# Kernel tuning notes

Hardware: AMD Instinct MI355X
Metric: run time of the kernel (lower is better)

Reference implementation:

```python
import jax, jax.numpy as jnp
import numpy as np

ROUTING_ITERS = 3
EPS = 1e-8

def _squash_elem(s):
    # Faithful to torch squash with dim=-1 over a trailing size-1 axis: elementwise.
    sq = s * s
    return (sq / (1.0 + sq)) * s / jnp.sqrt(sq + EPS)

def setup_inputs() -> dict:
    key = jax.random.key(0)
    k1, k2 = jax.random.split(key)
    x = jax.random.normal(k1, (64, 1152, 64), dtype=jnp.float32)            # [B, N_routes, in_ch]
    route_weights = jax.random.normal(k2, (32, 1152, 64, 64), dtype=jnp.float32)  # [C, N, out, in]
    return {"x": x, "route_weights": route_weights}

def reference(x, route_weights):
    B = x.shape[0]
    C, N, O, _ = route_weights.shape
    # u_hat: [B, C, N, O]  (torch trailing size-1 dim dropped; squash/sums over it are elementwise)
    u_hat = jnp.einsum('cnoi,bni->bcno', route_weights, x)
    b_ij = jnp.zeros((B, C, N, 1), dtype=x.dtype)
    v_j = None
    for i in range(ROUTING_ITERS):
        c_ij = jax.nn.softmax(b_ij, axis=1)                  # over capsules
        s_j = jnp.sum(c_ij * u_hat, axis=2, keepdims=True)   # [B, C, 1, O]
        v_j = _squash_elem(s_j)
        if i < ROUTING_ITERS - 1:
            # torch: b_ij + (u_hat * v_j).sum(-1, keepdim) over size-1 dim -> broadcasts to [B,C,N,O]
            b_ij = b_ij + u_hat * v_j
    return v_j[:, :, 0, :]  # [B, C, O]
```

## Files before the change

kernel.cpp:

```cpp
#include <hip/hip_runtime.h>
#include <hip/hip_bf16.h>

typedef short short8v __attribute__((ext_vector_type(8)));
typedef float float4v __attribute__((ext_vector_type(4)));

constexpr int Bb = 64;
constexpr int Cc = 32;
constexpr int Nn = 1152;
constexpr int Oo = 64;
constexpr int Ii = 64;
constexpr int NCH = 32;
constexpr int CHN = 36;
constexpr int OT  = 16;

__device__ __forceinline__ unsigned short bf16_rne(float f) {
    unsigned u = __float_as_uint(f);
    u += 0x7FFFu + ((u >> 16) & 1u);
    return (unsigned short)(u >> 16);
}
__device__ __forceinline__ float bf16_f(unsigned short h) {
    return __uint_as_float(((unsigned)h) << 16);
}
__device__ __forceinline__ float squash_elem(float s) {
    float sq = s * s;
    return (sq / (1.f + sq)) * s / sqrtf(sq + 1e-8f);
}

__device__ __forceinline__ void barrier_nodrain() {
    asm volatile("s_waitcnt lgkmcnt(0)" ::: "memory");
    __builtin_amdgcn_s_barrier();
    asm volatile("" ::: "memory");
}

__device__ __forceinline__ void split8(const float4& f0, const float4& f1,
                                       short8v& h, short8v& lo) {
    float a[8] = {f0.x, f0.y, f0.z, f0.w, f1.x, f1.y, f1.z, f1.w};
#pragma unroll
    for (int e = 0; e < 8; ++e) {
        unsigned short hb = bf16_rne(a[e]);
        h[e] = (short)hb;
        lo[e] = (short)bf16_rne(a[e] - bf16_f(hb));
    }
}

__global__ __launch_bounds__(256) void prep_xt(const float* __restrict__ x,
                                               unsigned short* __restrict__ xh,
                                               unsigned short* __restrict__ xl) {
    const int n = blockIdx.x, t = threadIdx.x;
    const int b = t >> 2, q = t & 3;
    const float* src = x + ((size_t)b * Nn + n) * Ii + q * 16;
    float4 v0 = *(const float4*)(src);
    float4 v1 = *(const float4*)(src + 4);
    float4 v2 = *(const float4*)(src + 8);
    float4 v3 = *(const float4*)(src + 12);
    short8v h0, l0, h1, l1;
    split8(v0, v1, h0, l0);
    split8(v2, v3, h1, l1);
    size_t dst = (size_t)n * (Bb * Ii) + b * Ii + q * 16;
    *(short8v*)(xh + dst) = h0;
    *(short8v*)(xh + dst + 8) = h1;
    *(short8v*)(xl + dst) = l0;
    *(short8v*)(xl + dst + 8) = l1;
}

template <int MODE>
__global__ __launch_bounds__(256, 2) void caps_pass(
    const float* __restrict__ w, const unsigned short* __restrict__ xh,
    const unsigned short* __restrict__ xl, const float* __restrict__ V,
    float* __restrict__ part) {
    __shared__ unsigned short sh[2][128 * 64];
    __shared__ unsigned short sl[2][128 * 64];

    const int t = threadIdx.x;
    const int l = t & 63, wv = t >> 6;
    const int ch = blockIdx.x, ot = blockIdx.y;
    const int obase = ot * 4;
    const int kg = l >> 4;
    const int lm = l & 15;
    const int n0 = ch * CHN;
    const int sw = (lm & 7) << 3;

    float Vreg[8][4];
    if constexpr (MODE == 1) {
#pragma unroll
        for (int t8 = 0; t8 < 8; ++t8)
#pragma unroll
            for (int r = 0; r < 4; ++r) {
                int b = 16 * wv + 4 * kg + r;
                int c = 4 * t8 + ((l >> 2) & 3);
                int o = obase + (l & 3);
                Vreg[t8][r] = V[((size_t)b * Cc + c) * Oo + o];
            }
    }
    float4v acc4[8];
    float accs[8][4];
#pragma unroll
    for (int t8 = 0; t8 < 8; ++t8) {
        acc4[t8] = (float4v){0.f, 0.f, 0.f, 0.f};
#pragma unroll
        for (int r = 0; r < 4; ++r) accs[t8][r] = 0.f;
    }

    const int i0 = (t & 15) * 4;
    const int colb = t >> 4;
    float4 L0[8], L1[8];

    auto issue = [&](int n, float4(&ld)[8]) {
#pragma unroll
        for (int k = 0; k < 8; ++k) {
            int col = colb + 16 * k;
            int c = col >> 2, olc = col & 3;
            ld[k] = *(const float4*)(
                w + (((size_t)c * Nn + n) * Oo + obase + olc) * Ii + i0);
        }
    };
    auto writebuf = [&](unsigned short* dh, unsigned short* dl,
                        const float4(&ld)[8]) {
#pragma unroll
        for (int k = 0; k < 8; ++k) {
            int col = colb + 16 * k;
            int off = col * 64 + (i0 ^ ((col & 7) << 3));
            short8v H, Lo;
            split8(ld[k], *(const float4*)nullptr == *(const float4*)nullptr
                              ? ld[k]
                              : ld[k],
                   H, Lo);
        }
    };
    (void)writebuf;

    auto writebuf2 = [&](unsigned short* dh, unsigned short* dl,
                         const float4(&ld)[8]) {
#pragma unroll
        for (int k = 0; k < 8; ++k) {
            int col = colb + 16 * k;
            int off = col * 64 + (i0 ^ ((col & 7) << 3));
            float a[4] = {ld[k].x, ld[k].y, ld[k].z, ld[k].w};
            ushort4 H, L;
            unsigned short* hp = (unsigned short*)&H;
            unsigned short* lp = (unsigned short*)&L;
#pragma unroll
            for (int e = 0; e < 4; ++e) {
                unsigned short hb = bf16_rne(a[e]);
                hp[e] = hb;
                lp[e] = bf16_rne(a[e] - bf16_f(hb));
            }
            *(ushort4*)(dh + off) = H;
            *(ushort4*)(dl + off) = L;
        }
    };

    auto compute = [&](const unsigned short* bh_, const unsigned short* bl_,
                       int n) {
        const size_t xoff =
            (size_t)n * (Bb * Ii) + (16 * wv + lm) * Ii + kg * 8;
        short8v ah0 = *(const short8v*)(xh + xoff);
        short8v al0 = *(const short8v*)(xl + xoff);
        short8v ah1 = *(const short8v*)(xh + xoff + 32);
        short8v al1 = *(const short8v*)(xl + xoff + 32);

        float u[8][4];
#pragma unroll
        for (int t8 = 0; t8 < 8; ++t8) {
            int row = 16 * t8 + lm;
            int c0 = row * 64 + ((kg * 8) ^ sw);
            int c1 = row * 64 + (((kg * 8) + 32) ^ sw);
            short8v bh0 = *(const short8v*)(bh_ + c0);
            short8v bl0 = *(const short8v*)(bl_ + c0);
            short8v bh1 = *(const short8v*)(bh_ + c1);
            short8v bl1 = *(const short8v*)(bl_ + c1);
            float4v a;
            if constexpr (MODE == 0) a = acc4[t8];
            else a = (float4v){0.f, 0.f, 0.f, 0.f};
            a = __builtin_amdgcn_mfma_f32_16x16x32_bf16(ah0, bh0, a, 0, 0, 0);
            a = __builtin_amdgcn_mfma_f32_16x16x32_bf16(al0, bh0, a, 0, 0, 0);
            a = __builtin_amdgcn_mfma_f32_16x16x32_bf16(ah0, bl0, a, 0, 0, 0);
            a = __builtin_amdgcn_mfma_f32_16x16x32_bf16(ah1, bh1, a, 0, 0, 0);
            a = __builtin_amdgcn_mfma_f32_16x16x32_bf16(al1, bh1, a, 0, 0, 0);
            a = __builtin_amdgcn_mfma_f32_16x16x32_bf16(ah1, bl1, a, 0, 0, 0);
            if constexpr (MODE == 0) {
                acc4[t8] = a;
            } else {
                u[t8][0] = a[0]; u[t8][1] = a[1];
                u[t8][2] = a[2]; u[t8][3] = a[3];
            }
        }
        if constexpr (MODE == 1) {
#pragma unroll
            for (int r = 0; r < 4; ++r) {
                float m = -1e30f;
#pragma unroll
                for (int t8 = 0; t8 < 8; ++t8)
                    m = fmaxf(m, u[t8][r] * Vreg[t8][r]);
                m = fmaxf(m, __shfl_xor(m, 4));
                m = fmaxf(m, __shfl_xor(m, 8));
                float Z = 0.f;
#pragma unroll
                for (int t8 = 0; t8 < 8; ++t8) {
                    float e = __expf(u[t8][r] * Vreg[t8][r] - m);
                    Z += e;
                    u[t8][r] *= e;
                }
                Z += __shfl_xor(Z, 4);
                Z += __shfl_xor(Z, 8);
                float rz = 1.f / Z;
#pragma unroll
                for (int t8 = 0; t8 < 8; ++t8) accs[t8][r] += u[t8][r] * rz;
            }
        }
    };

    issue(n0, L0);
    writebuf2(sh[0], sl[0], L0);
    issue(n0 + 1, L1);
    barrier_nodrain();

    for (int j = 0; j < CHN; j += 2) {
        writebuf2(sh[1], sl[1], L1);
        if (j + 2 < CHN) issue(n0 + j + 2, L0);
        compute(sh[0], sl[0], n0 + j);
        barrier_nodrain();
        if (j + 2 < CHN) writebuf2(sh[0], sl[0], L0);
        if (j + 3 < CHN) issue(n0 + j + 3, L1);
        compute(sh[1], sl[1], n0 + j + 1);
        barrier_nodrain();
    }

#pragma unroll
    for (int t8 = 0; t8 < 8; ++t8)
#pragma unroll
        for (int r = 0; r < 4; ++r) {
            int b = 16 * wv + 4 * kg + r;
            int c = 4 * t8 + ((l >> 2) & 3);
            int o = obase + (l & 3);
            float val = (MODE == 0) ? acc4[t8][r] : accs[t8][r];
            part[(((size_t)ch * Bb + b) * Cc + c) * Oo + o] = val;
        }
}

__global__ void reduce_caps(const float* __restrict__ part,
                            float* __restrict__ V, float* __restrict__ out,
                            int mode) {
    int bc = blockIdx.x;
    int o = threadIdx.x;
    size_t base = (size_t)bc * 64 + o;
    float s = 0.f;
    for (int c = 0; c < NCH; ++c) s += part[(size_t)c * (Bb * Cc * Oo) + base];
    if (mode == 0)      V[base] = squash_elem(s * (1.f / 32.f));
    else if (mode == 1) V[base] += squash_elem(s);
    else                out[base] = squash_elem(s);
}

extern "C" void kernel_launch(void* const* d_in, const int* in_sizes, int n_in,
                              void* d_out, int out_size, void* d_ws, size_t ws_size,
                              hipStream_t stream) {
    const float* x = (const float*)d_in[0];
    const float* w = (const float*)d_in[1];
    float* out = (float*)d_out;

    const size_t XE = (size_t)Bb * Nn * Ii;
    unsigned short* xh = (unsigned short*)d_ws;
    unsigned short* xl = xh + XE;
    float* part = (float*)(xl + XE);
    float* V = part + (size_t)NCH * Bb * Cc * Oo;

    prep_xt<<<Nn, 256, 0, stream>>>(x, xh, xl);

    caps_pass<0><<<dim3(NCH, OT), 256, 0, stream>>>(w, xh, xl, nullptr, part);
    reduce_caps<<<Bb * Cc, 64, 0, stream>>>(part, V, out, 0);
    caps_pass<1><<<dim3(NCH, OT), 256, 0, stream>>>(w, xh, xl, V, part);
    reduce_caps<<<Bb * Cc, 64, 0, stream>>>(part, V, out, 1);
    caps_pass<1><<<dim3(NCH, OT), 256, 0, stream>>>(w, xh, xl, V, part);
    reduce_caps<<<Bb * Cc, 64, 0, stream>>>(part, V, out, 2);
}
```

Before: 496.4 us.

## Widen caps tile to 8 outputs per block with 512 threads and single-stage prefetch

Each block now covers 8 output channels instead of 4 using 8 waves. Pairs of waves share a batch group and split the output columns, which halves the grid and lets each x fragment load serve twice the weight columns. The pipeline becomes a simple per-step loop: one register staging buffer feeding double-buffered LDS, with a new XOR swizzle keyed on column bits. LDS use doubles to 128 KB per block, which may limit occupancy, and the single-stage prefetch gives less latency hiding.

```diff
diff --git a/kernel.cpp b/kernel.cpp
--- a/kernel.cpp
+++ b/kernel.cpp
@@ -11,7 +11,7 @@
 constexpr int Ii = 64;
 constexpr int NCH = 32;
 constexpr int CHN = 36;
-constexpr int OT  = 16;
+constexpr int OT  = 8;
 
 __device__ __forceinline__ unsigned short bf16_rne(float f) {
     unsigned u = __float_as_uint(f);
@@ -64,33 +64,31 @@
 }
 
 template <int MODE>
-__global__ __launch_bounds__(256, 2) void caps_pass(
+__global__ __launch_bounds__(512, 2) void caps_pass(
     const float* __restrict__ w, const unsigned short* __restrict__ xh,
     const unsigned short* __restrict__ xl, const float* __restrict__ V,
     float* __restrict__ part) {
-    __shared__ unsigned short sh[2][128 * 64];
-    __shared__ unsigned short sl[2][128 * 64];
+    __shared__ unsigned short sh[2][256 * 64];
+    __shared__ unsigned short sl[2][256 * 64];
 
     const int t = threadIdx.x;
     const int l = t & 63, wv = t >> 6;
+    const int bg = wv >> 1, q = wv & 1;
     const int ch = blockIdx.x, ot = blockIdx.y;
-    const int obase = ot * 4;
-    const int kg = l >> 4;
-    const int lm = l & 15;
+    const int obase = ot * 8;
+    const int kg = l >> 4, lm = l & 15;
+    const int cc = (l >> 2) & 3, ol3 = l & 3;
+    const int o = obase + 4 * q + ol3;
     const int n0 = ch * CHN;
-    const int sw = (lm & 7) << 3;
 
     float Vreg[8][4];
     if constexpr (MODE == 1) {
 #pragma unroll
         for (int t8 = 0; t8 < 8; ++t8)
 #pragma unroll
-            for (int r = 0; r < 4; ++r) {
-                int b = 16 * wv + 4 * kg + r;
-                int c = 4 * t8 + ((l >> 2) & 3);
-                int o = obase + (l & 3);
-                Vreg[t8][r] = V[((size_t)b * Cc + c) * Oo + o];
-            }
+            for (int r = 0; r < 4; ++r)
+                Vreg[t8][r] =
+                    V[((size_t)(16 * bg + 4 * kg + r) * Cc + 4 * t8 + cc) * Oo + o];
     }
     float4v acc4[8];
     float accs[8][4];
@@ -103,42 +101,27 @@
 
     const int i0 = (t & 15) * 4;
     const int colb = t >> 4;
-    float4 L0[8], L1[8];
-
-    auto issue = [&](int n, float4(&ld)[8]) {
+    float4 L[8];
+
+    auto issue = [&](int n) {
 #pragma unroll
         for (int k = 0; k < 8; ++k) {
-            int col = colb + 16 * k;
-            int c = col >> 2, olc = col & 3;
-            ld[k] = *(const float4*)(
+            int col = colb + 32 * k;
+            int c = col >> 3, olc = col & 7;
+            L[k] = *(const float4*)(
                 w + (((size_t)c * Nn + n) * Oo + obase + olc) * Ii + i0);
         }
     };
-    auto writebuf = [&](unsigned short* dh, unsigned short* dl,
-                        const float4(&ld)[8]) {
+    auto writebuf = [&](unsigned short* dh, unsigned short* dl) {
 #pragma unroll
         for (int k = 0; k < 8; ++k) {
-            int col = colb + 16 * k;
-            int off = col * 64 + (i0 ^ ((col & 7) << 3));
-            short8v H, Lo;
-            split8(ld[k], *(const float4*)nullptr == *(const float4*)nullptr
-                              ? ld[k]
-                              : ld[k],
-                   H, Lo);
-        }
-    };
-    (void)writebuf;
-
-    auto writebuf2 = [&](unsigned short* dh, unsigned short* dl,
-                         const float4(&ld)[8]) {
-#pragma unroll
-        for (int k = 0; k < 8; ++k) {
-            int col = colb + 16 * k;
-            int off = col * 64 + (i0 ^ ((col & 7) << 3));
-            float a[4] = {ld[k].x, ld[k].y, ld[k].z, ld[k].w};
-            ushort4 H, L;
+            int col = colb + 32 * k;
+            int key = (col & 3) | (((col >> 3) & 1) << 2);
+            int off = col * 64 + (i0 ^ (key << 3));
+            float a[4] = {L[k].x, L[k].y, L[k].z, L[k].w};
+            ushort4 H, Lo;
             unsigned short* hp = (unsigned short*)&H;
-            unsigned short* lp = (unsigned short*)&L;
+            unsigned short* lp = (unsigned short*)&Lo;
 #pragma unroll
             for (int e = 0; e < 4; ++e) {
                 unsigned short hb = bf16_rne(a[e]);
@@ -146,14 +129,14 @@
                 lp[e] = bf16_rne(a[e] - bf16_f(hb));
             }
             *(ushort4*)(dh + off) = H;
-            *(ushort4*)(dl + off) = L;
+            *(ushort4*)(dl + off) = Lo;
         }
     };
 
     auto compute = [&](const unsigned short* bh_, const unsigned short* bl_,
                        int n) {
         const size_t xoff =
-            (size_t)n * (Bb * Ii) + (16 * wv + lm) * Ii + kg * 8;
+            (size_t)n * (Bb * Ii) + (16 * bg + lm) * Ii + kg * 8;
         short8v ah0 = *(const short8v*)(xh + xoff);
         short8v al0 = *(const short8v*)(xl + xoff);
         short8v ah1 = *(const short8v*)(xh + xoff + 32);
@@ -162,13 +145,14 @@
         float u[8][4];
 #pragma unroll
         for (int t8 = 0; t8 < 8; ++t8) {
-            int row = 16 * t8 + lm;
-            int c0 = row * 64 + ((kg * 8) ^ sw);
-            int c1 = row * 64 + (((kg * 8) + 32) ^ sw);
-            short8v bh0 = *(const short8v*)(bh_ + c0);
-            short8v bl0 = *(const short8v*)(bl_ + c0);
-            short8v bh1 = *(const short8v*)(bh_ + c1);
-            short8v bl1 = *(const short8v*)(bl_ + c1);
+            int col = 32 * t8 + 8 * cc + 4 * q + ol3;
+            int key = ol3 | ((cc & 1) << 2);
+            int off0 = col * 64 + 8 * (kg ^ key);
+            int off1 = col * 64 + 8 * ((kg + 4) ^ key);
+            short8v bh0 = *(const short8v*)(bh_ + off0);
+            short8v bl0 = *(const short8v*)(bl_ + off0);
+            short8v bh1 = *(const short8v*)(bh_ + off1);
+            short8v bl1 = *(const short8v*)(bl_ + off1);
             float4v a;
             if constexpr (MODE == 0) a = acc4[t8];
             else a = (float4v){0.f, 0.f, 0.f, 0.f};
@@ -210,29 +194,21 @@
         }
     };
 
-    issue(n0, L0);
-    writebuf2(sh[0], sl[0], L0);
-    issue(n0 + 1, L1);
-    barrier_nodrain();
-
-    for (int j = 0; j < CHN; j += 2) {
-        writebuf2(sh[1], sl[1], L1);
-        if (j + 2 < CHN) issue(n0 + j + 2, L0);
-        compute(sh[0], sl[0], n0 + j);
+    issue(n0);
+    for (int j = 0; j < CHN; ++j) {
+        const int cur = j & 1;
+        writebuf(sh[cur], sl[cur]);
+        if (j + 1 < CHN) issue(n0 + j + 1);
         barrier_nodrain();
-        if (j + 2 < CHN) writebuf2(sh[0], sl[0], L0);
-        if (j + 3 < CHN) issue(n0 + j + 3, L1);
-        compute(sh[1], sl[1], n0 + j + 1);
-        barrier_nodrain();
+        compute(sh[cur], sl[cur], n0 + j);
     }
 
 #pragma unroll
     for (int t8 = 0; t8 < 8; ++t8)
 #pragma unroll
         for (int r = 0; r < 4; ++r) {
-            int b = 16 * wv + 4 * kg + r;
-            int c = 4 * t8 + ((l >> 2) & 3);
-            int o = obase + (l & 3);
+            int b = 16 * bg + 4 * kg + r;
+            int c = 4 * t8 + cc;
             float val = (MODE == 0) ? acc4[t8][r] : accs[t8][r];
             part[(((size_t)ch * Bb + b) * Cc + c) * Oo + o] = val;
         }
@@ -266,10 +242,10 @@
 
     prep_xt<<<Nn, 256, 0, stream>>>(x, xh, xl);
 
-    caps_pass<0><<<dim3(NCH, OT), 256, 0, stream>>>(w, xh, xl, nullptr, part);
+    caps_pass<0><<<dim3(NCH, OT), 512, 0, stream>>>(w, xh, xl, nullptr, part);
     reduce_caps<<<Bb * Cc, 64, 0, stream>>>(part, V, out, 0);
-    caps_pass<1><<<dim3(NCH, OT), 256, 0, stream>>>(w, xh, xl, V, part);
+    caps_pass<1><<<dim3(NCH, OT), 512, 0, stream>>>(w, xh, xl, V, part);
     reduce_caps<<<Bb * Cc, 64, 0, stream>>>(part, V, out, 1);
-    caps_pass<1><<<dim3(NCH, OT), 256, 0, stream>>>(w, xh, xl, V, part);
+    caps_pass<1><<<dim3(NCH, OT), 512, 0, stream>>>(w, xh, xl, V, part);
     reduce_caps<<<Bb * Cc, 64, 0, stream>>>(part, V, out, 2);
 }
```

Result: slower. 544.4 us (+9.7%).
